# Optimization experiments

Hardware: AMD Instinct MI355X
Metric: run time of the kernel (lower is better)

Reference implementation:

```python
import jax, jax.numpy as jnp
import numpy as np

ALPHA = 0.2  # leaky_relu negative slope
NFEAT = 3    # node_feat_size for final tanh slice


def _init_linear(key, out_f, in_f):
    kw, kb = jax.random.split(key)
    scale = 1.0 / np.sqrt(in_f)
    w = jax.random.uniform(kw, (out_f, in_f), jnp.float32, -scale, scale)
    b = jax.random.uniform(kb, (out_f,), jnp.float32, -scale, scale)
    return w, b


def setup_inputs() -> dict:
    key = jax.random.key(0)
    ks = jax.random.split(key, 8)
    B, N, H = 64, 100, 32
    inp = {"x": jax.random.normal(ks[0], (B, N, H), jnp.float32)}
    # fe: [65 -> 96 -> 160 -> 192]; fn: [224 -> 256 -> 256 -> 32]
    fe_dims = [(96, 65), (160, 96), (192, 160)]
    fn_dims = [(256, 224), (256, 256), (32, 256)]
    for i, (o, f) in enumerate(fe_dims):
        w, b = _init_linear(ks[1 + i], o, f)
        inp[f"fe_w{i}"] = w
        inp[f"fe_b{i}"] = b
    for i, (o, f) in enumerate(fn_dims):
        w, b = _init_linear(ks[4 + i], o, f)
        inp[f"fn_w{i}"] = w
        inp[f"fn_b{i}"] = b
    return inp


def _forward(x, fe_params, fn_params):
    B, N, H = x.shape
    # --- getA: all-pairs edge features (pos_diffs) ---
    x1 = jnp.broadcast_to(x[:, :, None, :], (B, N, N, H))  # sender i
    x2 = jnp.broadcast_to(x[:, None, :, :], (B, N, N, H))  # receiver j
    dists = jnp.linalg.norm(x2[..., :2] - x1[..., :2] + 1e-12, axis=-1, keepdims=True)
    A = jnp.concatenate([x1, x2, dists], axis=-1)  # [B,N,N,2H+1]
    # --- edge MLP (all layers with leaky_relu) ---
    for w, b in fe_params:
        A = jax.nn.leaky_relu(jnp.einsum("bijf,of->bijo", A, w) + b, ALPHA)
    # sum-aggregate over neighbor axis j
    A = jnp.sum(A, axis=2)  # [B,N,fe_out]
    # --- node MLP (leaky_relu on all but last) ---
    h = jnp.concatenate([A, x], axis=-1)  # [B,N,fe_out+H]
    for w, b in fn_params[:-1]:
        h = jax.nn.leaky_relu(jnp.einsum("bnf,of->bno", h, w) + b, ALPHA)
    w, b = fn_params[-1]
    h = jnp.einsum("bnf,of->bno", h, w) + b  # [B,N,H]
    return jnp.tanh(h[..., :NFEAT])


def reference(x, fe_w0, fe_b0, fe_w1, fe_b1, fe_w2, fe_b2,
              fn_w0, fn_b0, fn_w1, fn_b1, fn_w2, fn_b2):
    fe_params = [(fe_w0, fe_b0), (fe_w1, fe_b1), (fe_w2, fe_b2)]
    fn_params = [(fn_w0, fn_b0), (fn_w1, fn_b1), (fn_w2, fn_b2)]
    return _forward(x, fe_params, fn_params)
```

## Files before the change

### kernel.cpp

```cpp
#include <hip/hip_runtime.h>
#include <hip/hip_bf16.h>
#include <math.h>

#define ALPHA 0.2f

typedef __attribute__((ext_vector_type(8))) short bf16x8;
typedef __attribute__((ext_vector_type(4))) float f32x4;

static __device__ __forceinline__ float lrelu(float v) {
    return v > 0.0f ? v : ALPHA * v;
}
static __device__ __forceinline__ uint16_t f2b(float f) {
    union { float f; uint32_t u; } c; c.f = f;
    const uint32_t u = c.u + 0x7FFFu + ((c.u >> 16) & 1u);
    return (uint16_t)(u >> 16);
}
static __device__ __forceinline__ float b2f16(uint16_t h) {
    union { uint32_t u; float f; } c; c.u = ((uint32_t)h) << 16; return c.f;
}

__global__ __launch_bounds__(256) void convert_weights(
    const float* __restrict__ w0, const float* __restrict__ w1,
    const float* __restrict__ w2, const float* __restrict__ f0,
    const float* __restrict__ f1,
    uint16_t* __restrict__ o0, float* __restrict__ od,
    uint16_t* __restrict__ o1, uint16_t* __restrict__ o2,
    uint16_t* __restrict__ of0, uint16_t* __restrict__ of1)
{
    const int t0 = blockIdx.x * 256 + threadIdx.x;
    const int stride = gridDim.x * 256;
    for (int t = t0; t < 96 * 32; t += stride) {
        const int n = t >> 5, k = t & 31;
        o0[t] = f2b(w0[n * 65 + 32 + k]);
    }
    for (int t = t0; t < 96; t += stride) od[t] = w0[t * 65 + 64];
    for (int t = t0; t < 160 * 96; t += stride) o1[t] = f2b(w1[t]);
    for (int t = t0; t < 192 * 160; t += stride) o2[t] = f2b(w2[t]);
    for (int t = t0; t < 256 * 224; t += stride) of0[t] = f2b(f0[t]);
    for (int t = t0; t < 256 * 256; t += stride) of1[t] = f2b(f1[t]);
}

__global__ __launch_bounds__(256, 3) void edge_kernel(
    const float* __restrict__ x,
    const float* __restrict__ w0f, const float* __restrict__ b0f,
    const float* __restrict__ b1f, const float* __restrict__ eb2,
    const uint16_t* __restrict__ wb0p, const float* __restrict__ wd0,
    const uint16_t* __restrict__ wb1, const uint16_t* __restrict__ wb2,
    float* __restrict__ hin)
{
    __shared__ __align__(16) uint16_t R1[64 * 168];
    __shared__ __align__(16) uint16_t R2[112 * 104];
    __shared__ __align__(16) float base0[96];
    __shared__ __align__(16) float dist[112];

    const int bi = blockIdx.x;
    const int b = bi / 100, i = bi % 100;
    const int t = threadIdx.x;
    const int lane = t & 63, wave = t >> 6;
    const int col = lane & 15, g = lane >> 4;

    float* xb = (float*)R2;
    const float* xg = x + (size_t)b * 3200;
    for (int idx = t; idx < 3200; idx += 256)
        xb[(idx >> 5) * 33 + (idx & 31)] = xg[idx];
    __syncthreads();

    float* hinrow = hin + (size_t)bi * 256;
    if (t < 32) hinrow[192 + t] = xb[i * 33 + t];
    if (t < 96) {
        const float* wr = w0f + t * 65;
        float a = b0f[t];
#pragma unroll
        for (int k = 0; k < 32; ++k) a += wr[k] * xb[i * 33 + k];
        base0[t] = a;
    }
    if (t < 112) {
        float d = 0.0f;
        if (t < 100) {
            const float dx = xb[t * 33 + 0] - xb[i * 33 + 0] + 1e-12f;
            const float dy = xb[t * 33 + 1] - xb[i * 33 + 1] + 1e-12f;
            d = sqrtf(dx * dx + dy * dy);
        }
        dist[t] = d;
    }
    for (int idx = t; idx < 112 * 32; idx += 256) {
        const int r = idx >> 5, k = idx & 31;
        R1[r * 40 + k] = f2b(r < 100 ? xb[r * 33 + k] : 0.0f);
    }
    __syncthreads();

    {
        f32x4 acc[2][7];
#pragma unroll
        for (int s = 0; s < 2; ++s) {
            const int nt = wave + 4 * s;
            if (nt < 6) {
                const float bv = base0[nt * 16 + col];
                const float wdv = wd0[nt * 16 + col];
                const bf16x8 bfr = *(const bf16x8*)(wb0p + (nt * 16 + col) * 32 + 8 * g);
#pragma unroll
                for (int m = 0; m < 7; ++m) {
                    acc[s][m] = (f32x4){bv, bv, bv, bv};
                    const bf16x8 af = *(const bf16x8*)(R1 + (m * 16 + col) * 40 + 8 * g);
                    acc[s][m] = __builtin_amdgcn_mfma_f32_16x16x32_bf16(af, bfr, acc[s][m], 0, 0, 0);
                    const f32x4 dq = *(const f32x4*)(dist + m * 16 + 4 * g);
#pragma unroll
                    for (int r = 0; r < 4; ++r) acc[s][m][r] += wdv * dq[r];
                }
            }
        }
#pragma unroll
        for (int s = 0; s < 2; ++s) {
            const int nt = wave + 4 * s;
            if (nt < 6) {
#pragma unroll
                for (int m = 0; m < 7; ++m)
#pragma unroll
                    for (int r = 0; r < 4; ++r)
                        R2[(m * 16 + 4 * g + r) * 104 + nt * 16 + col] =
                            f2b(lrelu(acc[s][m][r]));
            }
        }
    }
    __syncthreads();

    float ssum[3] = {0.f, 0.f, 0.f};
#pragma unroll
    for (int sub = 0; sub < 2; ++sub) {
        const int MT = (sub == 0) ? 4 : 3;
        {
            f32x4 acc[3][4];
#pragma unroll
            for (int s = 0; s < 3; ++s) {
                const int nt = wave + 4 * s;
                if (nt < 10) {
                    const float bv = b1f[nt * 16 + col];
#pragma unroll
                    for (int m = 0; m < 4; ++m) if (m < MT)
                        acc[s][m] = (f32x4){bv, bv, bv, bv};
#pragma unroll
                    for (int kt = 0; kt < 3; ++kt) {
                        const bf16x8 bfr = *(const bf16x8*)(
                            wb1 + (size_t)(nt * 16 + col) * 96 + kt * 32 + 8 * g);
#pragma unroll
                        for (int m = 0; m < 4; ++m) if (m < MT) {
                            const bf16x8 af = *(const bf16x8*)(
                                R2 + ((sub * 4 + m) * 16 + col) * 104 + kt * 32 + 8 * g);
                            acc[s][m] = __builtin_amdgcn_mfma_f32_16x16x32_bf16(
                                af, bfr, acc[s][m], 0, 0, 0);
                        }
                    }
#pragma unroll
                    for (int m = 0; m < 4; ++m) if (m < MT)
#pragma unroll
                        for (int r = 0; r < 4; ++r)
                            R1[(m * 16 + 4 * g + r) * 168 + nt * 16 + col] =
                                f2b(lrelu(acc[s][m][r]));
                }
            }
        }
        __syncthreads();
        {
            f32x4 acc[3][4];
#pragma unroll
            for (int s = 0; s < 3; ++s) {
                const int nt = wave + 4 * s;
                const float bv = eb2[nt * 16 + col];
#pragma unroll
                for (int m = 0; m < 4; ++m) if (m < MT)
                    acc[s][m] = (f32x4){bv, bv, bv, bv};
#pragma unroll
                for (int kt = 0; kt < 5; ++kt) {
                    const bf16x8 bfr = *(const bf16x8*)(
                        wb2 + (size_t)(nt * 16 + col) * 160 + kt * 32 + 8 * g);
#pragma unroll
                    for (int m = 0; m < 4; ++m) if (m < MT) {
                        const bf16x8 af = *(const bf16x8*)(
                            R1 + (m * 16 + col) * 168 + kt * 32 + 8 * g);
                        acc[s][m] = __builtin_amdgcn_mfma_f32_16x16x32_bf16(
                            af, bfr, acc[s][m], 0, 0, 0);
                    }
                }
                float ps = 0.0f;
#pragma unroll
                for (int m = 0; m < 4; ++m) if (m < MT) {
                    const bool needmask = (sub == 1 && m == 2);
                    const int rowbase = sub * 64 + m * 16 + 4 * g;
#pragma unroll
                    for (int r = 0; r < 4; ++r) {
                        if (!needmask || (rowbase + r < 100))
                            ps += lrelu(acc[s][m][r]);
                    }
                }
                ssum[s] += ps;
            }
        }
        if (sub == 0) __syncthreads();
    }
#pragma unroll
    for (int s = 0; s < 3; ++s) {
        float v = ssum[s];
        v += __shfl_xor(v, 16);
        v += __shfl_xor(v, 32);
        if (lane < 16) hinrow[(wave + 4 * s) * 16 + col] = v;
    }
}

__global__ __launch_bounds__(256) void node_kernel(
    const float* __restrict__ hin,
    const uint16_t* __restrict__ wfn0, const float* __restrict__ fb0,
    const uint16_t* __restrict__ wfn1, const float* __restrict__ fb1,
    const float* __restrict__ fw2, const float* __restrict__ fb2,
    float* __restrict__ out)
{
    __shared__ __align__(16) uint16_t RA[16 * 264];
    __shared__ __align__(16) uint16_t RH[16 * 264];
    const int t = threadIdx.x, lane = t & 63, wave = t >> 6;
    const int col = lane & 15, g = lane >> 4;
    const int r0 = blockIdx.x * 16;

    for (int r = wave; r < 16; r += 4) {
        const float* src = hin + (size_t)(r0 + r) * 256;
        for (int c = lane; c < 224; c += 64)
            RA[r * 232 + c] = f2b(src[c]);
    }
    __syncthreads();

    {
        f32x4 acc[4];
#pragma unroll
        for (int s = 0; s < 4; ++s) {
            const float bv = fb0[(wave + 4 * s) * 16 + col];
            acc[s] = (f32x4){bv, bv, bv, bv};
        }
#pragma unroll
        for (int kt = 0; kt < 7; ++kt) {
            const bf16x8 af = *(const bf16x8*)(RA + col * 232 + kt * 32 + 8 * g);
#pragma unroll
            for (int s = 0; s < 4; ++s) {
                const int nt = wave + 4 * s;
                const bf16x8 bfr = *(const bf16x8*)(
                    wfn0 + (size_t)(nt * 16 + col) * 224 + kt * 32 + 8 * g);
                acc[s] = __builtin_amdgcn_mfma_f32_16x16x32_bf16(af, bfr, acc[s], 0, 0, 0);
            }
        }
#pragma unroll
        for (int s = 0; s < 4; ++s) {
            const int nt = wave + 4 * s;
#pragma unroll
            for (int r = 0; r < 4; ++r)
                RH[(4 * g + r) * 264 + nt * 16 + col] = f2b(lrelu(acc[s][r]));
        }
    }
    __syncthreads();
    {
        f32x4 acc[4];
#pragma unroll
        for (int s = 0; s < 4; ++s) {
            const float bv = fb1[(wave + 4 * s) * 16 + col];
            acc[s] = (f32x4){bv, bv, bv, bv};
        }
#pragma unroll
        for (int kt = 0; kt < 8; ++kt) {
            const bf16x8 af = *(const bf16x8*)(RH + col * 264 + kt * 32 + 8 * g);
#pragma unroll
            for (int s = 0; s < 4; ++s) {
                const int nt = wave + 4 * s;
                const bf16x8 bfr = *(const bf16x8*)(
                    wfn1 + (size_t)(nt * 16 + col) * 256 + kt * 32 + 8 * g);
                acc[s] = __builtin_amdgcn_mfma_f32_16x16x32_bf16(af, bfr, acc[s], 0, 0, 0);
            }
        }
        __syncthreads();
#pragma unroll
        for (int s = 0; s < 4; ++s) {
            const int nt = wave + 4 * s;
#pragma unroll
            for (int r = 0; r < 4; ++r)
                RA[(4 * g + r) * 264 + nt * 16 + col] = f2b(lrelu(acc[s][r]));
        }
    }
    __syncthreads();
    const int row = t >> 4, u = t & 15;
    float h = 0.0f;
    if (u < 12) {
        const int o = u >> 2, ks = u & 3;
        const float* w = fw2 + o * 256 + ks * 64;
        const uint16_t* hr = RA + row * 264 + ks * 64;
        float a = 0.0f;
#pragma unroll 8
        for (int k = 0; k < 64; k += 4) {
            const ushort4 hv = *(const ushort4*)(hr + k);
            a += w[k + 0] * b2f16(hv.x) + w[k + 1] * b2f16(hv.y)
               + w[k + 2] * b2f16(hv.z) + w[k + 3] * b2f16(hv.w);
        }
        h = a;
    }
    h += __shfl_xor(h, 1);
    h += __shfl_xor(h, 2);
    if (u < 12 && (u & 3) == 0) {
        const int o = u >> 2;
        out[(size_t)(r0 + row) * 3 + o] = tanhf(h + fb2[o]);
    }
}

extern "C" void kernel_launch(void* const* d_in, const int* in_sizes, int n_in,
                              void* d_out, int out_size, void* d_ws, size_t ws_size,
                              hipStream_t stream) {
    (void)in_sizes; (void)n_in; (void)out_size; (void)ws_size;
    const float* x     = (const float*)d_in[0];
    const float* fe_w0 = (const float*)d_in[1];
    const float* fe_b0 = (const float*)d_in[2];
    const float* fe_w1 = (const float*)d_in[3];
    const float* fe_b1 = (const float*)d_in[4];
    const float* fe_w2 = (const float*)d_in[5];
    const float* fe_b2 = (const float*)d_in[6];
    const float* fn_w0 = (const float*)d_in[7];
    const float* fn_b0 = (const float*)d_in[8];
    const float* fn_w1 = (const float*)d_in[9];
    const float* fn_b1 = (const float*)d_in[10];
    const float* fn_w2 = (const float*)d_in[11];
    const float* fn_b2 = (const float*)d_in[12];
    float* out = (float*)d_out;

    float* buf0 = (float*)d_ws;
    uint16_t* wq   = (uint16_t*)(buf0 + (size_t)6400 * 256);
    uint16_t* wb0p = wq;
    uint16_t* wb1  = wb0p + 96 * 32;
    uint16_t* wb2  = wb1 + 160 * 96;
    uint16_t* wfn0 = wb2 + 192 * 160;
    uint16_t* wfn1 = wfn0 + 256 * 224;
    float*    wd0  = (float*)(wfn1 + 256 * 256);

    convert_weights<<<64, 256, 0, stream>>>(fe_w0, fe_w1, fe_w2, fn_w0, fn_w1,
                                            wb0p, wd0, wb1, wb2, wfn0, wfn1);
    edge_kernel<<<6400, 256, 0, stream>>>(x, fe_w0, fe_b0, fe_b1, fe_b2,
                                          wb0p, wd0, wb1, wb2, buf0);
    node_kernel<<<400, 256, 0, stream>>>(buf0, wfn0, fn_b0, wfn1, fn_b1,
                                         fn_w2, fn_b2, out);
}
```

Before: 166.3 us.

## Factor first edge layer into per-node precompute and restructure edge MLP tiling

The first edge-MLP layer is linear in the concatenated sender and receiver features, so it is split into per-node sender terms (base0T) and receiver terms (GT). A new precompute kernel produces these once per node, along with the xy coordinates and the x copy into the node input buffer. The edge kernel now builds layer-1 activations by adding these terms plus the distance contribution, replacing the per-edge MFMA with elementwise work. It also processes rows in 48-row chunks with a smaller shared-memory footprint, raises the occupancy hint to 4 blocks, reorders MFMA loops to reuse weight fragments, and adds s_setprio around the MFMA sections. The cost is extra global traffic for the precomputed GT and base0T tensors and layer-1 accumulation in fp32 before the bf16 conversion.

Result: slower. 415.1 us (+149.6%).

```diff
diff --git a/kernel.cpp b/kernel.cpp
--- a/kernel.cpp
+++ b/kernel.cpp
@@ -1,5 +1,4 @@
 #include <hip/hip_runtime.h>
-#include <hip/hip_bf16.h>
 #include <math.h>
 
 #define ALPHA 0.2f
@@ -15,187 +14,191 @@
     const uint32_t u = c.u + 0x7FFFu + ((c.u >> 16) & 1u);
     return (uint16_t)(u >> 16);
 }
+static __device__ __forceinline__ uint32_t pk2(float a, float b) {
+    return (uint32_t)f2b(a) | ((uint32_t)f2b(b) << 16);
+}
 static __device__ __forceinline__ float b2f16(uint16_t h) {
     union { uint32_t u; float f; } c; c.u = ((uint32_t)h) << 16; return c.f;
 }
 
-__global__ __launch_bounds__(256) void convert_weights(
-    const float* __restrict__ w0, const float* __restrict__ w1,
+__global__ __launch_bounds__(256) void precompute(
+    const float* __restrict__ x, const float* __restrict__ w0,
+    const float* __restrict__ b0, const float* __restrict__ w1,
     const float* __restrict__ w2, const float* __restrict__ f0,
     const float* __restrict__ f1,
-    uint16_t* __restrict__ o0, float* __restrict__ od,
-    uint16_t* __restrict__ o1, uint16_t* __restrict__ o2,
-    uint16_t* __restrict__ of0, uint16_t* __restrict__ of1)
+    float* __restrict__ base0T, float* __restrict__ GT,
+    float* __restrict__ xyt, float* __restrict__ wd0,
+    uint16_t* __restrict__ wb1, uint16_t* __restrict__ wb2,
+    uint16_t* __restrict__ wfn0, uint16_t* __restrict__ wfn1,
+    float* __restrict__ hin)
 {
-    const int t0 = blockIdx.x * 256 + threadIdx.x;
-    const int stride = gridDim.x * 256;
-    for (int t = t0; t < 96 * 32; t += stride) {
-        const int n = t >> 5, k = t & 31;
-        o0[t] = f2b(w0[n * 65 + 32 + k]);
-    }
-    for (int t = t0; t < 96; t += stride) od[t] = w0[t * 65 + 64];
-    for (int t = t0; t < 160 * 96; t += stride) o1[t] = f2b(w1[t]);
-    for (int t = t0; t < 192 * 160; t += stride) o2[t] = f2b(w2[t]);
-    for (int t = t0; t < 256 * 224; t += stride) of0[t] = f2b(f0[t]);
-    for (int t = t0; t < 256 * 256; t += stride) of1[t] = f2b(f1[t]);
-}
-
-__global__ __launch_bounds__(256, 3) void edge_kernel(
-    const float* __restrict__ x,
-    const float* __restrict__ w0f, const float* __restrict__ b0f,
+    const int blk = blockIdx.x, t = threadIdx.x;
+    if (blk >= 100) {
+        const int t0 = (blk - 100) * 256 + t;
+        for (int i = t0; i < 160 * 96;  i += 7168) wb1[i]  = f2b(w1[i]);
+        for (int i = t0; i < 192 * 160; i += 7168) wb2[i]  = f2b(w2[i]);
+        for (int i = t0; i < 256 * 224; i += 7168) wfn0[i] = f2b(f0[i]);
+        for (int i = t0; i < 256 * 256; i += 7168) wfn1[i] = f2b(f1[i]);
+        if (t0 < 96) wd0[t0] = w0[t0 * 65 + 64];
+        return;
+    }
+    __shared__ float W0s[96 * 65];
+    __shared__ float xs[64 * 32];
+    const int r0 = blk * 64;
+    for (int i = t; i < 96 * 65; i += 256) W0s[i] = w0[i];
+    for (int i = t; i < 2048; i += 256) xs[i] = x[(size_t)r0 * 32 + i];
+    __syncthreads();
+    for (int it = 0; it < 48; ++it) {
+        const int out = t + 256 * it;
+        const int row = out / 192, oi = out - row * 192;
+        const int o = (oi < 96) ? oi : oi - 96;
+        const float* wr = W0s + o * 65 + ((oi < 96) ? 0 : 32);
+        const float* xr = xs + row * 32;
+        float a = (oi < 96) ? b0[o] : 0.0f;
+#pragma unroll
+        for (int k = 0; k < 32; ++k) a += wr[k] * xr[k];
+        if (oi < 96) base0T[(size_t)(r0 + row) * 96 + o] = a;
+        else         GT[(size_t)(r0 + row) * 96 + o] = a;
+    }
+    for (int i = t; i < 128; i += 256)
+        xyt[(r0 + (i >> 1)) * 2 + (i & 1)] = xs[(i >> 1) * 32 + (i & 1)];
+    for (int i = t; i < 2048; i += 256)
+        hin[(size_t)(r0 + (i >> 5)) * 256 + 192 + (i & 31)] = xs[i];
+}
+
+__global__ __launch_bounds__(256, 4) void edge_kernel(
+    const float* __restrict__ base0T, const float* __restrict__ GT,
+    const float* __restrict__ xyt, const float* __restrict__ wd0,
     const float* __restrict__ b1f, const float* __restrict__ eb2,
-    const uint16_t* __restrict__ wb0p, const float* __restrict__ wd0,
     const uint16_t* __restrict__ wb1, const uint16_t* __restrict__ wb2,
     float* __restrict__ hin)
 {
-    __shared__ __align__(16) uint16_t R1[64 * 168];
-    __shared__ __align__(16) uint16_t R2[112 * 104];
-    __shared__ __align__(16) float base0[96];
-    __shared__ __align__(16) float dist[112];
-
-    const int bi = blockIdx.x;
-    const int b = bi / 100, i = bi % 100;
+    __shared__ __align__(16) uint16_t H1[112 * 104];
+    __shared__ __align__(16) uint16_t H2l[48 * 168];
+    __shared__ __align__(16) float b0wd[192];
+
+    const int bi = blockIdx.x, b = bi / 100;
     const int t = threadIdx.x;
     const int lane = t & 63, wave = t >> 6;
     const int col = lane & 15, g = lane >> 4;
 
-    float* xb = (float*)R2;
-    const float* xg = x + (size_t)b * 3200;
-    for (int idx = t; idx < 3200; idx += 256)
-        xb[(idx >> 5) * 33 + (idx & 31)] = xg[idx];
+    if (t < 96) b0wd[t] = base0T[(size_t)bi * 96 + t];
+    else if (t < 192) b0wd[t] = wd0[t - 96];
+    const float xix = xyt[bi * 2 + 0], xiy = xyt[bi * 2 + 1];
+    __syncthreads();
+
+    for (int it = 0; it < 11; ++it) {
+        const int q = t + 256 * it;
+        if (q < 2688) {
+            const int j = q / 24, o4 = q - j * 24;
+            uint32_t lo = 0, hi = 0;
+            if (j < 100) {
+                const float4 gv = *(const float4*)(GT + (size_t)(b * 100 + j) * 96 + o4 * 4);
+                const float2 p = *(const float2*)(xyt + (b * 100 + j) * 2);
+                const float dx = p.x - xix + 1e-12f, dy = p.y - xiy + 1e-12f;
+                const float d = sqrtf(dx * dx + dy * dy);
+                const float4 bb = *(const float4*)(b0wd + o4 * 4);
+                const float4 wv = *(const float4*)(b0wd + 96 + o4 * 4);
+                lo = pk2(lrelu(gv.x + bb.x + wv.x * d), lrelu(gv.y + bb.y + wv.y * d));
+                hi = pk2(lrelu(gv.z + bb.z + wv.z * d), lrelu(gv.w + bb.w + wv.w * d));
+            }
+            *(uint2*)(H1 + j * 104 + o4 * 4) = (uint2){lo, hi};
+        }
+    }
     __syncthreads();
 
     float* hinrow = hin + (size_t)bi * 256;
-    if (t < 32) hinrow[192 + t] = xb[i * 33 + t];
-    if (t < 96) {
-        const float* wr = w0f + t * 65;
-        float a = b0f[t];
-#pragma unroll
-        for (int k = 0; k < 32; ++k) a += wr[k] * xb[i * 33 + k];
-        base0[t] = a;
-    }
-    if (t < 112) {
-        float d = 0.0f;
-        if (t < 100) {
-            const float dx = xb[t * 33 + 0] - xb[i * 33 + 0] + 1e-12f;
-            const float dy = xb[t * 33 + 1] - xb[i * 33 + 1] + 1e-12f;
-            d = sqrtf(dx * dx + dy * dy);
-        }
-        dist[t] = d;
-    }
-    for (int idx = t; idx < 112 * 32; idx += 256) {
-        const int r = idx >> 5, k = idx & 31;
-        R1[r * 40 + k] = f2b(r < 100 ? xb[r * 33 + k] : 0.0f);
-    }
-    __syncthreads();
-
-    {
-        f32x4 acc[2][7];
-#pragma unroll
-        for (int s = 0; s < 2; ++s) {
-            const int nt = wave + 4 * s;
-            if (nt < 6) {
-                const float bv = base0[nt * 16 + col];
-                const float wdv = wd0[nt * 16 + col];
-                const bf16x8 bfr = *(const bf16x8*)(wb0p + (nt * 16 + col) * 32 + 8 * g);
-#pragma unroll
-                for (int m = 0; m < 7; ++m) {
-                    acc[s][m] = (f32x4){bv, bv, bv, bv};
-                    const bf16x8 af = *(const bf16x8*)(R1 + (m * 16 + col) * 40 + 8 * g);
-                    acc[s][m] = __builtin_amdgcn_mfma_f32_16x16x32_bf16(af, bfr, acc[s][m], 0, 0, 0);
-                    const f32x4 dq = *(const f32x4*)(dist + m * 16 + 4 * g);
-#pragma unroll
-                    for (int r = 0; r < 4; ++r) acc[s][m][r] += wdv * dq[r];
-                }
-            }
-        }
-#pragma unroll
-        for (int s = 0; s < 2; ++s) {
-            const int nt = wave + 4 * s;
-            if (nt < 6) {
-#pragma unroll
-                for (int m = 0; m < 7; ++m)
-#pragma unroll
-                    for (int r = 0; r < 4; ++r)
-                        R2[(m * 16 + 4 * g + r) * 104 + nt * 16 + col] =
-                            f2b(lrelu(acc[s][m][r]));
-            }
-        }
-    }
-    __syncthreads();
-
     float ssum[3] = {0.f, 0.f, 0.f};
 #pragma unroll
-    for (int sub = 0; sub < 2; ++sub) {
-        const int MT = (sub == 0) ? 4 : 3;
+    for (int sub = 0; sub < 3; ++sub) {
+        const int MT = (sub < 2) ? 3 : 1;
         {
-            f32x4 acc[3][4];
+            f32x4 acc[3][3];
 #pragma unroll
             for (int s = 0; s < 3; ++s) {
                 const int nt = wave + 4 * s;
                 if (nt < 10) {
                     const float bv = b1f[nt * 16 + col];
 #pragma unroll
-                    for (int m = 0; m < 4; ++m) if (m < MT)
+                    for (int m = 0; m < 3; ++m) if (m < MT)
                         acc[s][m] = (f32x4){bv, bv, bv, bv};
-#pragma unroll
-                    for (int kt = 0; kt < 3; ++kt) {
-                        const bf16x8 bfr = *(const bf16x8*)(
-                            wb1 + (size_t)(nt * 16 + col) * 96 + kt * 32 + 8 * g);
-#pragma unroll
-                        for (int m = 0; m < 4; ++m) if (m < MT) {
-                            const bf16x8 af = *(const bf16x8*)(
-                                R2 + ((sub * 4 + m) * 16 + col) * 104 + kt * 32 + 8 * g);
-                            acc[s][m] = __builtin_amdgcn_mfma_f32_16x16x32_bf16(
-                                af, bfr, acc[s][m], 0, 0, 0);
-                        }
+                }
+            }
+            __builtin_amdgcn_s_setprio(1);
+#pragma unroll
+            for (int kt = 0; kt < 3; ++kt) {
+                bf16x8 bfr[3];
+#pragma unroll
+                for (int s = 0; s < 3; ++s) {
+                    const int nt = wave + 4 * s;
+                    if (nt < 10)
+                        bfr[s] = *(const bf16x8*)(wb1 + (size_t)(nt * 16 + col) * 96 + kt * 32 + 8 * g);
+                }
+#pragma unroll
+                for (int m = 0; m < 3; ++m) if (m < MT) {
+                    const bf16x8 af = *(const bf16x8*)(H1 + (sub * 48 + m * 16 + col) * 104 + kt * 32 + 8 * g);
+#pragma unroll
+                    for (int s = 0; s < 3; ++s) {
+                        const int nt = wave + 4 * s;
+                        if (nt < 10)
+                            acc[s][m] = __builtin_amdgcn_mfma_f32_16x16x32_bf16(af, bfr[s], acc[s][m], 0, 0, 0);
                     }
-#pragma unroll
-                    for (int m = 0; m < 4; ++m) if (m < MT)
+                }
+            }
+            __builtin_amdgcn_s_setprio(0);
+#pragma unroll
+            for (int s = 0; s < 3; ++s) {
+                const int nt = wave + 4 * s;
+                if (nt < 10) {
+#pragma unroll
+                    for (int m = 0; m < 3; ++m) if (m < MT)
 #pragma unroll
                         for (int r = 0; r < 4; ++r)
-                            R1[(m * 16 + 4 * g + r) * 168 + nt * 16 + col] =
+                            H2l[(m * 16 + 4 * g + r) * 168 + nt * 16 + col] =
                                 f2b(lrelu(acc[s][m][r]));
                 }
             }
         }
         __syncthreads();
         {
-            f32x4 acc[3][4];
+            f32x4 acc[3][3];
 #pragma unroll
             for (int s = 0; s < 3; ++s) {
-                const int nt = wave + 4 * s;
-                const float bv = eb2[nt * 16 + col];
-#pragma unroll
-                for (int m = 0; m < 4; ++m) if (m < MT)
+                const float bv = eb2[(wave + 4 * s) * 16 + col];
+#pragma unroll
+                for (int m = 0; m < 3; ++m) if (m < MT)
                     acc[s][m] = (f32x4){bv, bv, bv, bv};
-#pragma unroll
-                for (int kt = 0; kt < 5; ++kt) {
-                    const bf16x8 bfr = *(const bf16x8*)(
-                        wb2 + (size_t)(nt * 16 + col) * 160 + kt * 32 + 8 * g);
-#pragma unroll
-                    for (int m = 0; m < 4; ++m) if (m < MT) {
-                        const bf16x8 af = *(const bf16x8*)(
-                            R1 + (m * 16 + col) * 168 + kt * 32 + 8 * g);
-                        acc[s][m] = __builtin_amdgcn_mfma_f32_16x16x32_bf16(
-                            af, bfr, acc[s][m], 0, 0, 0);
-                    }
-                }
+            }
+            __builtin_amdgcn_s_setprio(1);
+#pragma unroll
+            for (int kt = 0; kt < 5; ++kt) {
+                bf16x8 bfr[3];
+#pragma unroll
+                for (int s = 0; s < 3; ++s)
+                    bfr[s] = *(const bf16x8*)(wb2 + (size_t)((wave + 4 * s) * 16 + col) * 160 + kt * 32 + 8 * g);
+#pragma unroll
+                for (int m = 0; m < 3; ++m) if (m < MT) {
+                    const bf16x8 af = *(const bf16x8*)(H2l + (m * 16 + col) * 168 + kt * 32 + 8 * g);
+#pragma unroll
+                    for (int s = 0; s < 3; ++s)
+                        acc[s][m] = __builtin_amdgcn_mfma_f32_16x16x32_bf16(af, bfr[s], acc[s][m], 0, 0, 0);
+                }
+            }
+            __builtin_amdgcn_s_setprio(0);
+#pragma unroll
+            for (int s = 0; s < 3; ++s) {
                 float ps = 0.0f;
 #pragma unroll
-                for (int m = 0; m < 4; ++m) if (m < MT) {
-                    const bool needmask = (sub == 1 && m == 2);
-                    const int rowbase = sub * 64 + m * 16 + 4 * g;
-#pragma unroll
-                    for (int r = 0; r < 4; ++r) {
-                        if (!needmask || (rowbase + r < 100))
-                            ps += lrelu(acc[s][m][r]);
-                    }
+                for (int m = 0; m < 3; ++m) if (m < MT) {
+                    const int rowbase = sub * 48 + m * 16 + 4 * g;
+#pragma unroll
+                    for (int r = 0; r < 4; ++r)
+                        if (sub < 2 || (rowbase + r < 100)) ps += lrelu(acc[s][m][r]);
                 }
                 ssum[s] += ps;
             }
         }
-        if (sub == 0) __syncthreads();
+        if (sub < 2) __syncthreads();
     }
 #pragma unroll
     for (int s = 0; s < 3; ++s) {
@@ -225,7 +228,6 @@
             RA[r * 232 + c] = f2b(src[c]);
     }
     __syncthreads();
-
     {
         f32x4 acc[4];
 #pragma unroll
@@ -238,19 +240,16 @@
             const bf16x8 af = *(const bf16x8*)(RA + col * 232 + kt * 32 + 8 * g);
 #pragma unroll
             for (int s = 0; s < 4; ++s) {
-                const int nt = wave + 4 * s;
                 const bf16x8 bfr = *(const bf16x8*)(
-                    wfn0 + (size_t)(nt * 16 + col) * 224 + kt * 32 + 8 * g);
+                    wfn0 + (size_t)((wave + 4 * s) * 16 + col) * 224 + kt * 32 + 8 * g);
                 acc[s] = __builtin_amdgcn_mfma_f32_16x16x32_bf16(af, bfr, acc[s], 0, 0, 0);
             }
         }
 #pragma unroll
-        for (int s = 0; s < 4; ++s) {
-            const int nt = wave + 4 * s;
+        for (int s = 0; s < 4; ++s)
 #pragma unroll
             for (int r = 0; r < 4; ++r)
-                RH[(4 * g + r) * 264 + nt * 16 + col] = f2b(lrelu(acc[s][r]));
-        }
+                RH[(4 * g + r) * 264 + (wave + 4 * s) * 16 + col] = f2b(lrelu(acc[s][r]));
     }
     __syncthreads();
     {
@@ -265,20 +264,17 @@
             const bf16x8 af = *(const bf16x8*)(RH + col * 264 + kt * 32 + 8 * g);
 #pragma unroll
             for (int s = 0; s < 4; ++s) {
-                const int nt = wave + 4 * s;
                 const bf16x8 bfr = *(const bf16x8*)(
-                    wfn1 + (size_t)(nt * 16 + col) * 256 + kt * 32 + 8 * g);
+                    wfn1 + (size_t)((wave + 4 * s) * 16 + col) * 256 + kt * 32 + 8 * g);
                 acc[s] = __builtin_amdgcn_mfma_f32_16x16x32_bf16(af, bfr, acc[s], 0, 0, 0);
             }
         }
         __syncthreads();
 #pragma unroll
-        for (int s = 0; s < 4; ++s) {
-            const int nt = wave + 4 * s;
+        for (int s = 0; s < 4; ++s)
 #pragma unroll
             for (int r = 0; r < 4; ++r)
-                RA[(4 * g + r) * 264 + nt * 16 + col] = f2b(lrelu(acc[s][r]));
-        }
+                RA[(4 * g + r) * 264 + (wave + 4 * s) * 16 + col] = f2b(lrelu(acc[s][r]));
     }
     __syncthreads();
     const int row = t >> 4, u = t & 15;
@@ -298,10 +294,8 @@
     }
     h += __shfl_xor(h, 1);
     h += __shfl_xor(h, 2);
-    if (u < 12 && (u & 3) == 0) {
-        const int o = u >> 2;
-        out[(size_t)(r0 + row) * 3 + o] = tanhf(h + fb2[o]);
-    }
+    if (u < 12 && (u & 3) == 0)
+        out[(size_t)(r0 + row) * 3 + (u >> 2)] = tanhf(h + fb2[u >> 2]);
 }
 
 extern "C" void kernel_launch(void* const* d_in, const int* in_sizes, int n_in,
@@ -323,19 +317,22 @@
     const float* fn_b2 = (const float*)d_in[12];
     float* out = (float*)d_out;
 
-    float* buf0 = (float*)d_ws;
-    uint16_t* wq   = (uint16_t*)(buf0 + (size_t)6400 * 256);
-    uint16_t* wb0p = wq;
-    uint16_t* wb1  = wb0p + 96 * 32;
+    float* buf0   = (float*)d_ws;
+    float* base0T = buf0 + (size_t)6400 * 256;
+    float* GT     = base0T + 6400 * 96;
+    float* xyt    = GT + 6400 * 96;
+    float* wd0    = xyt + 12800;
+    uint16_t* wb1  = (uint16_t*)(wd0 + 128);
     uint16_t* wb2  = wb1 + 160 * 96;
     uint16_t* wfn0 = wb2 + 192 * 160;
     uint16_t* wfn1 = wfn0 + 256 * 224;
-    float*    wd0  = (float*)(wfn1 + 256 * 256);
-
-    convert_weights<<<64, 256, 0, stream>>>(fe_w0, fe_w1, fe_w2, fn_w0, fn_w1,
-                                            wb0p, wd0, wb1, wb2, wfn0, wfn1);
-    edge_kernel<<<6400, 256, 0, stream>>>(x, fe_w0, fe_b0, fe_b1, fe_b2,
-                                          wb0p, wd0, wb1, wb2, buf0);
+
+    precompute<<<128, 256, 0, stream>>>(x, fe_w0, fe_b0, fe_w1, fe_w2,
+                                        fn_w0, fn_w1,
+                                        base0T, GT, xyt, wd0,
+                                        wb1, wb2, wfn0, wfn1, buf0);
+    edge_kernel<<<6400, 256, 0, stream>>>(base0T, GT, xyt, wd0,
+                                          fe_b1, fe_b2, wb1, wb2, buf0);
     node_kernel<<<400, 256, 0, stream>>>(buf0, wfn0, fn_b0, wfn1, fn_b1,
                                          fn_w2, fn_b2, out);
 }
```
